# Performance work log

Hardware: AMD Instinct MI355X
Metric: run time of the kernel (lower is better)

Reference implementation:

```python
import jax, jax.numpy as jnp
import numpy as np

N_NODES = 50000
N_EDGES = 625000
DIM = 128
DROPOUT_P = 0.5


def setup_inputs() -> dict:
    key = jax.random.key(0)
    kx, ke, kw, kb = jax.random.split(key, 4)
    x = jax.random.normal(kx, (N_NODES, DIM), dtype=jnp.float32)
    edge_index = jax.random.randint(ke, (2, N_EDGES), 0, N_NODES, dtype=jnp.int64)
    # GCNConv linear weight (glorot-ish) and bias
    W = jax.random.normal(kw, (DIM, DIM), dtype=jnp.float32) / np.sqrt(DIM)
    b = jnp.zeros((DIM,), dtype=jnp.float32)
    return {"x": x, "edge_index": edge_index, "W": W, "b": b}


def reference(x, edge_index, W, b):
    N = x.shape[0]
    # --- add self-loops ---
    loop = jnp.arange(N, dtype=edge_index.dtype)
    src = jnp.concatenate([edge_index[0], loop])  # [E+N]
    dst = jnp.concatenate([edge_index[1], loop])  # [E+N]
    # --- symmetric normalization: deg computed on destination nodes ---
    deg = jax.ops.segment_sum(jnp.ones_like(src, dtype=x.dtype), dst, num_segments=N)
    dis = jnp.where(deg > 0, jax.lax.rsqrt(jnp.where(deg > 0, deg, 1.0)), 0.0)
    norm = dis[src] * dis[dst]  # [E+N]
    # --- linear transform, gather, scatter-add ---
    h = x @ W  # [N, D]
    msg = h[src] * norm[:, None]  # [E+N, D]
    out = jax.ops.segment_sum(msg, dst, num_segments=N) + b  # [N, D]
    # --- ReLU + dropout (training mode, fixed key) + residual ---
    out = jax.nn.relu(out)
    keep = jax.random.bernoulli(jax.random.key(42), 1.0 - DROPOUT_P, out.shape)
    out = jnp.where(keep, out / (1.0 - DROPOUT_P), 0.0)
    out = out + x  # residual: input_dim == output_dim
    return out
```

## Files before the change

kernel.cpp:

```cpp
#include <hip/hip_runtime.h>
#include <hip/hip_bf16.h>
#include <stdint.h>

#define NDIM 128
#define LDK 136
#define BSH 9
#define NB_A 1024
#define BCAP 9216

typedef __attribute__((ext_vector_type(8))) short bf16x8;
typedef __attribute__((ext_vector_type(4))) float f32x4;

__device__ __forceinline__ unsigned short f2bf(float f) {
    unsigned u = __float_as_uint(f);
    unsigned r = u + 0x7fffu + ((u >> 16) & 1u);
    return (unsigned short)(r >> 16);
}
__device__ __forceinline__ float bf2f(unsigned short s) {
    return __uint_as_float(((unsigned)s) << 16);
}

__device__ __forceinline__ void load_edge(const unsigned* __restrict__ w, int is64, int E,
                                          int e, int& s, int& d) {
    if (is64) {
        s = (int)w[(size_t)2 * e];
        d = (int)w[(size_t)2 * E + (size_t)2 * e];
    } else {
        s = (int)w[e];
        d = (int)w[(size_t)E + e];
    }
}

__global__ void detect_kernel(const unsigned* __restrict__ w, int* flag) {
    __shared__ int any_nonzero;
    if (threadIdx.x == 0) any_nonzero = 0;
    __syncthreads();
    int nz = 0;
    for (int k = threadIdx.x; k < 2048; k += 256) {
        if (w[2 * k + 1] != 0u) nz = 1;
    }
    if (nz) atomicOr(&any_nonzero, 1);
    __syncthreads();
    if (threadIdx.x == 0) *flag = any_nonzero ? 0 : 1;
}

__global__ __launch_bounds__(256) void hist_kernel(const unsigned* __restrict__ w,
                                                   const int* __restrict__ flag,
                                                   int* __restrict__ hist,
                                                   int E, int nbuck, int chunk) {
    __shared__ int h[128];
    int t = threadIdx.x;
    if (t < 128) h[t] = 0;
    __syncthreads();
    int is64 = *flag;
    int lo = blockIdx.x * chunk;
    int hi = lo + chunk; if (hi > E) hi = E;
    for (int e = lo + t; e < hi; e += 256) {
        int s, d; load_edge(w, is64, E, e, s, d);
        atomicAdd(&h[d >> BSH], 1);
    }
    __syncthreads();
    if (t < nbuck) hist[(size_t)t * gridDim.x + blockIdx.x] = h[t];
}

__global__ __launch_bounds__(1024) void scanhist_kernel(int* __restrict__ hist,
                                                        int* __restrict__ btot, int NB) {
    __shared__ int s[1024];
    int t = threadIdx.x;
    size_t base = (size_t)blockIdx.x * NB;
    int v = hist[base + t];
    s[t] = v;
    __syncthreads();
    for (int d = 1; d < 1024; d <<= 1) {
        int add = (t >= d) ? s[t - d] : 0;
        __syncthreads();
        s[t] += add;
        __syncthreads();
    }
    hist[base + t] = s[t] - v;
    if (t == 1023) btot[blockIdx.x] = s[1023];
}

__global__ __launch_bounds__(128) void scanbuck_kernel(const int* __restrict__ btot,
                                                       int* __restrict__ bbase, int nbuck,
                                                       int* __restrict__ off, int N, int E) {
    __shared__ int s[128];
    int t = threadIdx.x;
    int v = (t < nbuck) ? btot[t] : 0;
    s[t] = v;
    __syncthreads();
    for (int d = 1; d < 128; d <<= 1) {
        int add = (t >= d) ? s[t - d] : 0;
        __syncthreads();
        s[t] += add;
        __syncthreads();
    }
    if (t < nbuck) bbase[t] = s[t] - v;
    if (t == 0) off[N] = E;
}

__global__ __launch_bounds__(256) void bucket_kernel(const unsigned* __restrict__ w,
                                                     const int* __restrict__ flag,
                                                     const int* __restrict__ hist,
                                                     const int* __restrict__ bbase,
                                                     unsigned* __restrict__ ebuf,
                                                     int E, int nbuck, int chunk) {
    __shared__ int cur[128];
    int t = threadIdx.x;
    if (t < nbuck) cur[t] = bbase[t] + hist[(size_t)t * gridDim.x + blockIdx.x];
    __syncthreads();
    int is64 = *flag;
    int lo = blockIdx.x * chunk;
    int hi = lo + chunk; if (hi > E) hi = E;
    for (int e = lo + t; e < hi; e += 256) {
        int s, d; load_edge(w, is64, E, e, s, d);
        int b = d >> BSH;
        int p = atomicAdd(&cur[b], 1);
        ebuf[p] = ((unsigned)s << BSH) | (unsigned)(d & ((1 << BSH) - 1));
    }
}

__global__ __launch_bounds__(512) void csr_kernel(const unsigned* __restrict__ ebuf,
                                                  const int* __restrict__ bbase,
                                                  const int* __restrict__ btot,
                                                  int* __restrict__ adj,
                                                  int* __restrict__ off,
                                                  float* __restrict__ dis,
                                                  int N) {
    __shared__ int lcnt[512];
    __shared__ int lscan[512];
    __shared__ int cur[512];
    __shared__ int tile[BCAP];
    int b = blockIdx.x, t = threadIdx.x;
    int start = bbase[b], cnt = btot[b];
    lcnt[t] = 0;
    __syncthreads();
    for (int i = t; i < cnt; i += 512) atomicAdd(&lcnt[ebuf[start + i] & 511], 1);
    __syncthreads();
    int v = lcnt[t];
    lscan[t] = v;
    __syncthreads();
    for (int d = 1; d < 512; d <<= 1) {
        int add = (t >= d) ? lscan[t - d] : 0;
        __syncthreads();
        lscan[t] += add;
        __syncthreads();
    }
    int ex = lscan[t] - v;
    int node = (b << BSH) + t;
    if (node < N) {
        off[node] = start + ex;
        dis[node] = rsqrtf((float)(v + 1));
    }
    cur[t] = ex;
    __syncthreads();
    if (cnt <= BCAP) {
        for (int i = t; i < cnt; i += 512) {
            unsigned wo = ebuf[start + i];
            int p = atomicAdd(&cur[wo & 511], 1);
            tile[p] = (int)(wo >> BSH);
        }
        __syncthreads();
        for (int i = t; i < cnt; i += 512) adj[start + i] = tile[i];
    } else {
        for (int i = t; i < cnt; i += 512) {
            unsigned wo = ebuf[start + i];
            int p = atomicAdd(&cur[wo & 511], 1);
            adj[start + p] = (int)(wo >> BSH);
        }
    }
}

__global__ __launch_bounds__(256) void gemm_kernel(const float* __restrict__ x,
                                                   const float* __restrict__ W,
                                                   const float* __restrict__ dis,
                                                   unsigned short* __restrict__ hp, int N) {
    __shared__ unsigned short Wt[NDIM][LDK];
    int tid = threadIdx.x;
    for (int i = tid; i < NDIM * NDIM; i += 256) {
        int k = i >> 7, c = i & 127;
        Wt[c][k] = f2bf(W[i]);
    }
    __syncthreads();

    const int lane = tid & 63;
    const int wv = tid >> 6;
    const int rowbase = blockIdx.x * 64 + wv * 16;
    const int l15 = lane & 15;
    const int kg = lane >> 4;
    const int arow = rowbase + l15;

    bf16x8 a[4];
#pragma unroll
    for (int s = 0; s < 4; ++s) {
        bf16x8 tt;
        if (arow < N) {
            const float* p = x + (size_t)arow * NDIM + s * 32 + kg * 8;
            float4 f0 = *(const float4*)p;
            float4 f1 = *(const float4*)(p + 4);
            tt[0] = (short)f2bf(f0.x); tt[1] = (short)f2bf(f0.y);
            tt[2] = (short)f2bf(f0.z); tt[3] = (short)f2bf(f0.w);
            tt[4] = (short)f2bf(f1.x); tt[5] = (short)f2bf(f1.y);
            tt[6] = (short)f2bf(f1.z); tt[7] = (short)f2bf(f1.w);
        } else {
#pragma unroll
            for (int e = 0; e < 8; ++e) tt[e] = 0;
        }
        a[s] = tt;
    }

    f32x4 acc[8];
#pragma unroll
    for (int ct = 0; ct < 8; ++ct) acc[ct] = (f32x4){0.f, 0.f, 0.f, 0.f};

#pragma unroll
    for (int ct = 0; ct < 8; ++ct) {
#pragma unroll
        for (int s = 0; s < 4; ++s) {
            bf16x8 bb = *(const bf16x8*)&Wt[ct * 16 + l15][s * 32 + kg * 8];
            acc[ct] = __builtin_amdgcn_mfma_f32_16x16x32_bf16(a[s], bb, acc[ct], 0, 0, 0);
        }
    }

    const int r0 = rowbase + kg * 4;
    float dv[4];
#pragma unroll
    for (int j = 0; j < 4; ++j) dv[j] = (r0 + j < N) ? dis[r0 + j] : 0.f;
#pragma unroll
    for (int ct = 0; ct < 8; ++ct) {
        int col = ct * 16 + l15;
#pragma unroll
        for (int j = 0; j < 4; ++j) {
            int r = r0 + j;
            if (r < N) hp[(size_t)r * NDIM + col] = f2bf(acc[ct][j] * dv[j]);
        }
    }
}

__device__ __forceinline__ unsigned rotl32(unsigned v, int d) {
    return (v << d) | (v >> (32 - d));
}
__device__ __forceinline__ unsigned tf_bits(unsigned ctr) {
    unsigned x0 = 0u, x1 = ctr;
    const unsigned ks0 = 0u, ks1 = 42u, ks2 = 0u ^ 42u ^ 0x1BD11BDAu;
    x0 += ks0; x1 += ks1;
#define RND(r) { x0 += x1; x1 = rotl32(x1, (r)); x1 ^= x0; }
    RND(13) RND(15) RND(26) RND(6)   x0 += ks1; x1 += ks2 + 1u;
    RND(17) RND(29) RND(16) RND(24)  x0 += ks2; x1 += ks0 + 2u;
    RND(13) RND(15) RND(26) RND(6)   x0 += ks0; x1 += ks1 + 3u;
    RND(17) RND(29) RND(16) RND(24)  x0 += ks1; x1 += ks2 + 4u;
    RND(13) RND(15) RND(26) RND(6)   x0 += ks2; x1 += ks0 + 5u;
#undef RND
    return x0 ^ x1;
}

__global__ __launch_bounds__(256) void gather_kernel(const unsigned short* __restrict__ hp,
                                                     const float* __restrict__ x,
                                                     const int* __restrict__ off,
                                                     const int* __restrict__ adj,
                                                     const float* __restrict__ dis,
                                                     const float* __restrict__ b,
                                                     float* __restrict__ out, int N) {
    int wave = (int)((blockIdx.x * 256u + threadIdx.x) >> 6);
    if (wave >= N) return;
    const int lane = threadIdx.x & 63;
    const int node = wave;
    const float dn = dis[node];
    const int c0 = lane * 2;
    const unsigned short* hpc = hp + c0;

    unsigned hv = *(const unsigned*)(hpc + (size_t)node * NDIM);
    float ax0 = bf2f((unsigned short)hv), ay0 = bf2f((unsigned short)(hv >> 16));
    float ax1 = 0.f, ay1 = 0.f, ax2 = 0.f, ay2 = 0.f, ax3 = 0.f, ay3 = 0.f;

    int k0 = off[node], k1 = off[node + 1];
    int kbase = k0;
    while (kbase < k1) {
        int nb = k1 - kbase; if (nb > 64) nb = 64;
        int myadj = (kbase + lane < k1) ? adj[kbase + lane] : 0;
        int j = 0;
        for (; j + 4 <= nb; j += 4) {
            int s0 = __shfl(myadj, j);
            int s1 = __shfl(myadj, j + 1);
            int s2 = __shfl(myadj, j + 2);
            int s3 = __shfl(myadj, j + 3);
            unsigned v0 = *(const unsigned*)(hpc + (size_t)s0 * NDIM);
            unsigned v1 = *(const unsigned*)(hpc + (size_t)s1 * NDIM);
            unsigned v2 = *(const unsigned*)(hpc + (size_t)s2 * NDIM);
            unsigned v3 = *(const unsigned*)(hpc + (size_t)s3 * NDIM);
            ax0 += bf2f((unsigned short)v0); ay0 += bf2f((unsigned short)(v0 >> 16));
            ax1 += bf2f((unsigned short)v1); ay1 += bf2f((unsigned short)(v1 >> 16));
            ax2 += bf2f((unsigned short)v2); ay2 += bf2f((unsigned short)(v2 >> 16));
            ax3 += bf2f((unsigned short)v3); ay3 += bf2f((unsigned short)(v3 >> 16));
        }
        for (; j < nb; ++j) {
            int s = __shfl(myadj, j);
            unsigned v = *(const unsigned*)(hpc + (size_t)s * NDIM);
            ax0 += bf2f((unsigned short)v); ay0 += bf2f((unsigned short)(v >> 16));
        }
        kbase += nb;
    }

    float ax = (ax0 + ax1) + (ax2 + ax3);
    float ay = (ay0 + ay1) + (ay2 + ay3);

    float v0 = fmaxf(fmaf(dn, ax, b[c0]), 0.f);
    float v1 = fmaxf(fmaf(dn, ay, b[c0 + 1]), 0.f);

    unsigned i0 = (unsigned)(node * NDIM + c0);
    unsigned bb0 = tf_bits(i0);
    unsigned bb1 = tf_bits(i0 + 1u);
    v0 = (bb0 >> 31) ? 0.f : v0 * 2.f;
    v1 = (bb1 >> 31) ? 0.f : v1 * 2.f;

    float2 xr = ((const float2*)(x + (size_t)node * NDIM))[lane];
    float2 o;
    o.x = v0 + xr.x;
    o.y = v1 + xr.y;
    ((float2*)(out + (size_t)node * NDIM))[lane] = o;
}

extern "C" void kernel_launch(void* const* d_in, const int* in_sizes, int n_in,
                              void* d_out, int out_size, void* d_ws, size_t ws_size,
                              hipStream_t stream) {
    const float* x = (const float*)d_in[0];
    const unsigned* edge_w = (const unsigned*)d_in[1];
    const float* W = (const float*)d_in[2];
    const float* b = (const float*)d_in[3];
    float* out = (float*)d_out;

    const int N = in_sizes[0] / NDIM;
    const int E = in_sizes[1] / 2;
    const int nbuck = (N + (1 << BSH) - 1) >> BSH;
    const int chunk = (E + NB_A - 1) / NB_A;

    char* ws = (char*)d_ws;
    unsigned short* hp = (unsigned short*)ws;
    float* dis   = (float*)(ws + (size_t)N * NDIM * sizeof(short));
    int*   off   = (int*)((char*)dis + (size_t)N * sizeof(float));
    int*   adj   = (int*)((char*)off + (size_t)(N + 4) * sizeof(int));
    unsigned* ebuf = (unsigned*)((char*)adj + (size_t)E * sizeof(int));
    int*   hist  = (int*)((char*)ebuf + (size_t)E * sizeof(unsigned));
    int*   btot  = (int*)((char*)hist + (size_t)128 * NB_A * sizeof(int));
    int*   bbase = (int*)((char*)btot + (size_t)128 * sizeof(int));
    int*   flag  = (int*)((char*)bbase + (size_t)128 * sizeof(int));

    detect_kernel<<<1, 256, 0, stream>>>(edge_w, flag);
    hist_kernel<<<NB_A, 256, 0, stream>>>(edge_w, flag, hist, E, nbuck, chunk);
    scanhist_kernel<<<nbuck, 1024, 0, stream>>>(hist, btot, NB_A);
    scanbuck_kernel<<<1, 128, 0, stream>>>(btot, bbase, nbuck, off, N, E);
    bucket_kernel<<<NB_A, 256, 0, stream>>>(edge_w, flag, hist, bbase, ebuf, E, nbuck, chunk);
    csr_kernel<<<nbuck, 512, 0, stream>>>(ebuf, bbase, btot, adj, off, dis, N);

    gemm_kernel<<<(N + 63) / 64, 256, 0, stream>>>(x, W, dis, hp, N);

    gather_kernel<<<(N + 3) / 4, 256, 0, stream>>>(hp, x, off, adj, dis, b, out, N);
}
```

Measured before the change: 84.28 us.

## Process two nodes per wave in gather and make GEMM grid-stride persistent

```diff
diff --git a/kernel.cpp b/kernel.cpp
--- a/kernel.cpp
+++ b/kernel.cpp
@@ -174,7 +174,8 @@
 __global__ __launch_bounds__(256) void gemm_kernel(const float* __restrict__ x,
                                                    const float* __restrict__ W,
                                                    const float* __restrict__ dis,
-                                                   unsigned short* __restrict__ hp, int N) {
+                                                   unsigned short* __restrict__ hp,
+                                                   int N, int ntiles) {
     __shared__ unsigned short Wt[NDIM][LDK];
     int tid = threadIdx.x;
     for (int i = tid; i < NDIM * NDIM; i += 256) {
@@ -185,54 +186,57 @@
 
     const int lane = tid & 63;
     const int wv = tid >> 6;
-    const int rowbase = blockIdx.x * 64 + wv * 16;
     const int l15 = lane & 15;
     const int kg = lane >> 4;
-    const int arow = rowbase + l15;
-
-    bf16x8 a[4];
-#pragma unroll
-    for (int s = 0; s < 4; ++s) {
-        bf16x8 tt;
-        if (arow < N) {
-            const float* p = x + (size_t)arow * NDIM + s * 32 + kg * 8;
-            float4 f0 = *(const float4*)p;
-            float4 f1 = *(const float4*)(p + 4);
-            tt[0] = (short)f2bf(f0.x); tt[1] = (short)f2bf(f0.y);
-            tt[2] = (short)f2bf(f0.z); tt[3] = (short)f2bf(f0.w);
-            tt[4] = (short)f2bf(f1.x); tt[5] = (short)f2bf(f1.y);
-            tt[6] = (short)f2bf(f1.z); tt[7] = (short)f2bf(f1.w);
-        } else {
-#pragma unroll
-            for (int e = 0; e < 8; ++e) tt[e] = 0;
-        }
-        a[s] = tt;
-    }
-
-    f32x4 acc[8];
-#pragma unroll
-    for (int ct = 0; ct < 8; ++ct) acc[ct] = (f32x4){0.f, 0.f, 0.f, 0.f};
-
-#pragma unroll
-    for (int ct = 0; ct < 8; ++ct) {
+
+    for (int tile = blockIdx.x; tile < ntiles; tile += gridDim.x) {
+        const int rowbase = tile * 64 + wv * 16;
+        const int arow = rowbase + l15;
+
+        bf16x8 a[4];
 #pragma unroll
         for (int s = 0; s < 4; ++s) {
-            bf16x8 bb = *(const bf16x8*)&Wt[ct * 16 + l15][s * 32 + kg * 8];
-            acc[ct] = __builtin_amdgcn_mfma_f32_16x16x32_bf16(a[s], bb, acc[ct], 0, 0, 0);
-        }
-    }
-
-    const int r0 = rowbase + kg * 4;
-    float dv[4];
-#pragma unroll
-    for (int j = 0; j < 4; ++j) dv[j] = (r0 + j < N) ? dis[r0 + j] : 0.f;
-#pragma unroll
-    for (int ct = 0; ct < 8; ++ct) {
-        int col = ct * 16 + l15;
-#pragma unroll
-        for (int j = 0; j < 4; ++j) {
-            int r = r0 + j;
-            if (r < N) hp[(size_t)r * NDIM + col] = f2bf(acc[ct][j] * dv[j]);
+            bf16x8 tt;
+            if (arow < N) {
+                const float* p = x + (size_t)arow * NDIM + s * 32 + kg * 8;
+                float4 f0 = *(const float4*)p;
+                float4 f1 = *(const float4*)(p + 4);
+                tt[0] = (short)f2bf(f0.x); tt[1] = (short)f2bf(f0.y);
+                tt[2] = (short)f2bf(f0.z); tt[3] = (short)f2bf(f0.w);
+                tt[4] = (short)f2bf(f1.x); tt[5] = (short)f2bf(f1.y);
+                tt[6] = (short)f2bf(f1.z); tt[7] = (short)f2bf(f1.w);
+            } else {
+#pragma unroll
+                for (int e = 0; e < 8; ++e) tt[e] = 0;
+            }
+            a[s] = tt;
+        }
+
+        f32x4 acc[8];
+#pragma unroll
+        for (int ct = 0; ct < 8; ++ct) acc[ct] = (f32x4){0.f, 0.f, 0.f, 0.f};
+
+#pragma unroll
+        for (int ct = 0; ct < 8; ++ct) {
+#pragma unroll
+            for (int s = 0; s < 4; ++s) {
+                bf16x8 bb = *(const bf16x8*)&Wt[ct * 16 + l15][s * 32 + kg * 8];
+                acc[ct] = __builtin_amdgcn_mfma_f32_16x16x32_bf16(a[s], bb, acc[ct], 0, 0, 0);
+            }
+        }
+
+        const int r0 = rowbase + kg * 4;
+        float dv[4];
+#pragma unroll
+        for (int j = 0; j < 4; ++j) dv[j] = (r0 + j < N) ? dis[r0 + j] : 0.f;
+#pragma unroll
+        for (int ct = 0; ct < 8; ++ct) {
+            int col = ct * 16 + l15;
+#pragma unroll
+            for (int j = 0; j < 4; ++j) {
+                int r = r0 + j;
+                if (r < N) hp[(size_t)r * NDIM + col] = f2bf(acc[ct][j] * dv[j]);
+            }
         }
     }
 }
@@ -261,63 +265,87 @@
                                                      const float* __restrict__ dis,
                                                      const float* __restrict__ b,
                                                      float* __restrict__ out, int N) {
-    int wave = (int)((blockIdx.x * 256u + threadIdx.x) >> 6);
-    if (wave >= N) return;
-    const int lane = threadIdx.x & 63;
-    const int node = wave;
-    const float dn = dis[node];
-    const int c0 = lane * 2;
+    int wid = (int)((blockIdx.x * 256u + threadIdx.x) >> 6);
+    int lane = threadIdx.x & 63;
+    int half = lane >> 5;
+    int l32 = lane & 31;
+    int node = wid * 2 + half;
+    bool valid = node < N;
+    int nodec = valid ? node : N - 1;
+    const float dn = dis[nodec];
+    const int c0 = l32 * 4;
     const unsigned short* hpc = hp + c0;
 
-    unsigned hv = *(const unsigned*)(hpc + (size_t)node * NDIM);
-    float ax0 = bf2f((unsigned short)hv), ay0 = bf2f((unsigned short)(hv >> 16));
-    float ax1 = 0.f, ay1 = 0.f, ax2 = 0.f, ay2 = 0.f, ax3 = 0.f, ay3 = 0.f;
-
-    int k0 = off[node], k1 = off[node + 1];
-    int kbase = k0;
-    while (kbase < k1) {
-        int nb = k1 - kbase; if (nb > 64) nb = 64;
-        int myadj = (kbase + lane < k1) ? adj[kbase + lane] : 0;
+    unsigned ctr = (unsigned)(nodec * NDIM + c0);
+    unsigned bt0 = tf_bits(ctr);
+    unsigned bt1 = tf_bits(ctr + 1u);
+    unsigned bt2 = tf_bits(ctr + 2u);
+    unsigned bt3 = tf_bits(ctr + 3u);
+
+    uint2 hv = *(const uint2*)(hpc + (size_t)nodec * NDIM);
+    float a00 = bf2f((unsigned short)hv.x), a01 = bf2f((unsigned short)(hv.x >> 16));
+    float a02 = bf2f((unsigned short)hv.y), a03 = bf2f((unsigned short)(hv.y >> 16));
+    float a10 = 0.f, a11 = 0.f, a12 = 0.f, a13 = 0.f;
+    float a20 = 0.f, a21 = 0.f, a22 = 0.f, a23 = 0.f;
+    float a30 = 0.f, a31 = 0.f, a32 = 0.f, a33 = 0.f;
+
+    int k0 = valid ? off[nodec] : 0;
+    int k1 = valid ? off[nodec + 1] : 0;
+    int kb = k0;
+    const int sbase = half << 5;
+    while (kb < k1) {
+        int nb = k1 - kb; if (nb > 32) nb = 32;
+        int myadj = (kb + l32 < k1) ? adj[kb + l32] : 0;
         int j = 0;
         for (; j + 4 <= nb; j += 4) {
-            int s0 = __shfl(myadj, j);
-            int s1 = __shfl(myadj, j + 1);
-            int s2 = __shfl(myadj, j + 2);
-            int s3 = __shfl(myadj, j + 3);
-            unsigned v0 = *(const unsigned*)(hpc + (size_t)s0 * NDIM);
-            unsigned v1 = *(const unsigned*)(hpc + (size_t)s1 * NDIM);
-            unsigned v2 = *(const unsigned*)(hpc + (size_t)s2 * NDIM);
-            unsigned v3 = *(const unsigned*)(hpc + (size_t)s3 * NDIM);
-            ax0 += bf2f((unsigned short)v0); ay0 += bf2f((unsigned short)(v0 >> 16));
-            ax1 += bf2f((unsigned short)v1); ay1 += bf2f((unsigned short)(v1 >> 16));
-            ax2 += bf2f((unsigned short)v2); ay2 += bf2f((unsigned short)(v2 >> 16));
-            ax3 += bf2f((unsigned short)v3); ay3 += bf2f((unsigned short)(v3 >> 16));
+            int s0 = __shfl(myadj, sbase + j);
+            int s1 = __shfl(myadj, sbase + j + 1);
+            int s2 = __shfl(myadj, sbase + j + 2);
+            int s3 = __shfl(myadj, sbase + j + 3);
+            uint2 v0 = *(const uint2*)(hpc + (size_t)s0 * NDIM);
+            uint2 v1 = *(const uint2*)(hpc + (size_t)s1 * NDIM);
+            uint2 v2 = *(const uint2*)(hpc + (size_t)s2 * NDIM);
+            uint2 v3 = *(const uint2*)(hpc + (size_t)s3 * NDIM);
+            a00 += bf2f((unsigned short)v0.x); a01 += bf2f((unsigned short)(v0.x >> 16));
+            a02 += bf2f((unsigned short)v0.y); a03 += bf2f((unsigned short)(v0.y >> 16));
+            a10 += bf2f((unsigned short)v1.x); a11 += bf2f((unsigned short)(v1.x >> 16));
+            a12 += bf2f((unsigned short)v1.y); a13 += bf2f((unsigned short)(v1.y >> 16));
+            a20 += bf2f((unsigned short)v2.x); a21 += bf2f((unsigned short)(v2.x >> 16));
+            a22 += bf2f((unsigned short)v2.y); a23 += bf2f((unsigned short)(v2.y >> 16));
+            a30 += bf2f((unsigned short)v3.x); a31 += bf2f((unsigned short)(v3.x >> 16));
+            a32 += bf2f((unsigned short)v3.y); a33 += bf2f((unsigned short)(v3.y >> 16));
         }
         for (; j < nb; ++j) {
-            int s = __shfl(myadj, j);
-            unsigned v = *(const unsigned*)(hpc + (size_t)s * NDIM);
-            ax0 += bf2f((unsigned short)v); ay0 += bf2f((unsigned short)(v >> 16));
-        }
-        kbase += nb;
-    }
-
-    float ax = (ax0 + ax1) + (ax2 + ax3);
-    float ay = (ay0 + ay1) + (ay2 + ay3);
-
-    float v0 = fmaxf(fmaf(dn, ax, b[c0]), 0.f);
-    float v1 = fmaxf(fmaf(dn, ay, b[c0 + 1]), 0.f);
-
-    unsigned i0 = (unsigned)(node * NDIM + c0);
-    unsigned bb0 = tf_bits(i0);
-    unsigned bb1 = tf_bits(i0 + 1u);
-    v0 = (bb0 >> 31) ? 0.f : v0 * 2.f;
-    v1 = (bb1 >> 31) ? 0.f : v1 * 2.f;
-
-    float2 xr = ((const float2*)(x + (size_t)node * NDIM))[lane];
-    float2 o;
-    o.x = v0 + xr.x;
-    o.y = v1 + xr.y;
-    ((float2*)(out + (size_t)node * NDIM))[lane] = o;
+            int s = __shfl(myadj, sbase + j);
+            uint2 v = *(const uint2*)(hpc + (size_t)s * NDIM);
+            a00 += bf2f((unsigned short)v.x); a01 += bf2f((unsigned short)(v.x >> 16));
+            a02 += bf2f((unsigned short)v.y); a03 += bf2f((unsigned short)(v.y >> 16));
+        }
+        kb += nb;
+    }
+
+    float c0s = (a00 + a10) + (a20 + a30);
+    float c1s = (a01 + a11) + (a21 + a31);
+    float c2s = (a02 + a12) + (a22 + a32);
+    float c3s = (a03 + a13) + (a23 + a33);
+
+    float4 bb = *(const float4*)(b + c0);
+    float v0 = fmaxf(fmaf(dn, c0s, bb.x), 0.f);
+    float v1 = fmaxf(fmaf(dn, c1s, bb.y), 0.f);
+    float v2 = fmaxf(fmaf(dn, c2s, bb.z), 0.f);
+    float v3 = fmaxf(fmaf(dn, c3s, bb.w), 0.f);
+
+    v0 = (bt0 >> 31) ? 0.f : v0 * 2.f;
+    v1 = (bt1 >> 31) ? 0.f : v1 * 2.f;
+    v2 = (bt2 >> 31) ? 0.f : v2 * 2.f;
+    v3 = (bt3 >> 31) ? 0.f : v3 * 2.f;
+
+    if (valid) {
+        float4 xr = *(const float4*)(x + (size_t)node * NDIM + c0);
+        float4 o;
+        o.x = v0 + xr.x; o.y = v1 + xr.y; o.z = v2 + xr.z; o.w = v3 + xr.w;
+        *(float4*)(out + (size_t)node * NDIM + c0) = o;
+    }
 }
 
 extern "C" void kernel_launch(void* const* d_in, const int* in_sizes, int n_in,
@@ -333,6 +361,7 @@
     const int E = in_sizes[1] / 2;
     const int nbuck = (N + (1 << BSH) - 1) >> BSH;
     const int chunk = (E + NB_A - 1) / NB_A;
+    const int ntiles = (N + 63) / 64;
 
     char* ws = (char*)d_ws;
     unsigned short* hp = (unsigned short*)ws;
@@ -352,7 +381,8 @@
     bucket_kernel<<<NB_A, 256, 0, stream>>>(edge_w, flag, hist, bbase, ebuf, E, nbuck, chunk);
     csr_kernel<<<nbuck, 512, 0, stream>>>(ebuf, bbase, btot, adj, off, dis, N);
 
-    gemm_kernel<<<(N + 63) / 64, 256, 0, stream>>>(x, W, dis, hp, N);
-
-    gather_kernel<<<(N + 3) / 4, 256, 0, stream>>>(hp, x, off, adj, dis, b, out, N);
-}
+    gemm_kernel<<<391, 256, 0, stream>>>(x, W, dis, hp, N, ntiles);
+
+    int waves = (N + 1) / 2;
+    gather_kernel<<<(waves + 3) / 4, 256, 0, stream>>>(hp, x, off, adj, dis, b, out, N);
+}
```

Result: no change. 84.65 us (+0.4%).
